# Kernel optimization log

Measured on AMD Instinct MI355X. Metric: run time of the kernel, lower is better.

Reference implementation:

```python
import jax, jax.numpy as jnp
import numpy as np

M, K, N = 131072, 512, 512


def setup_inputs() -> dict:
    key = jax.random.key(0)
    k1, k2, k3, k4 = jax.random.split(key, 4)
    # Simulated int8 quantized values held in float32 (real kernel uses int8)
    x = jnp.round(jax.random.normal(k1, (M, K), dtype=jnp.float32) * 30.0)
    weight = jnp.round(jax.random.normal(k2, (N, K), dtype=jnp.float32) * 30.0)
    # per-token activation scale [M,1], per-output-channel weight scale [N]
    x_scale = jax.random.uniform(k3, (M, 1), dtype=jnp.float32, minval=1e-3, maxval=2e-2)
    weight_scale = jax.random.uniform(k4, (N,), dtype=jnp.float32, minval=1e-3, maxval=2e-2)
    return {"x": x, "x_scale": x_scale, "weight": weight, "weight_scale": weight_scale}


def reference(x, x_scale, weight, weight_scale):
    # gemm_a8w8(per_Token): out[m,n] = (sum_k x[m,k]*W[n,k]) * x_scale[m] * w_scale[n]
    acc = jnp.einsum('mk,nk->mn', x, weight)          # [M, N] int32-equivalent accum
    out = acc * x_scale * weight_scale[None, :]       # fused dequant scaling
    return out  # otype would be bf16 in the original; kept fp32 as reference baseline
```

## Files before the change

### kernel.cpp

```cpp
#include <hip/hip_runtime.h>
#include <hip/hip_bf16.h>
#include <stdint.h>

#define K_DIM 512
#define N_DIM 512
#define BM 64
#define BN 256
#define PHASE_K 64
#define PHASE_FLOATS (BM * PHASE_K)
#define NBUF 3

typedef __bf16 bf16x8 __attribute__((ext_vector_type(8)));
typedef float floatx4 __attribute__((ext_vector_type(4)));

__device__ __forceinline__ bf16x8 cvt8(float4 a, float4 b) {
    bf16x8 r;
    r[0] = (__bf16)a.x; r[1] = (__bf16)a.y; r[2] = (__bf16)a.z; r[3] = (__bf16)a.w;
    r[4] = (__bf16)b.x; r[5] = (__bf16)b.y; r[6] = (__bf16)b.z; r[7] = (__bf16)b.w;
    return r;
}

__global__ __launch_bounds__(512) void wconv_kernel(const float* __restrict__ w,
                                                    __bf16* __restrict__ wf) {
    int t = blockIdx.x * 512 + threadIdx.x;
    int lane = t & 63, slot = t >> 6;
    int n = ((slot >> 4) << 4) + (lane & 15);
    int k = ((slot & 15) << 5) + ((lane >> 4) << 3);
    const float* src = w + (size_t)n * K_DIM + k;
    float4 f0 = *(const float4*)src;
    float4 f1 = *(const float4*)(src + 4);
    *(bf16x8*)(wf + (size_t)t * 8) = cvt8(f0, f1);
}

__device__ __forceinline__ void stage_phase(const float* __restrict__ x,
                                            int rowBase, int kBase,
                                            float* ldsBuf, int wid, int lane) {
    #pragma unroll
    for (int i = 0; i < 2; ++i) {
        int sl = i * 8 + wid;
        int row = sl * 4 + (lane >> 4);
        int srcByte = ((lane & 15) << 4) ^ ((row & 7) << 4);
        const float* g = x + (size_t)(rowBase + row) * K_DIM + kBase + (srcByte >> 2);
        float* l = ldsBuf + sl * 256;
        __builtin_amdgcn_global_load_lds(
            (const __attribute__((address_space(1))) void*)g,
            (__attribute__((address_space(3))) void*)l, 16, 0, 0);
    }
}

__device__ __forceinline__ bf16x8 read_afrag(const float* ldsBuf, int mg, int rt,
                                             int kcl, int lane) {
    int row = mg * 32 + rt * 16 + (lane & 15);
    int sw = (row & 7) << 4;
    int b0 = kcl * 128 + ((lane >> 4) << 5);
    const char* rb = (const char*)(ldsBuf + row * PHASE_K);
    float4 fa = *(const float4*)(rb + (b0 ^ sw));
    float4 fb = *(const float4*)(rb + ((b0 + 16) ^ sw));
    return cvt8(fa, fb);
}

template <bool USE_WF>
__device__ __forceinline__ void load_wfrag(bf16x8 (&dst)[4][2], int p,
                                           const __bf16* __restrict__ wf,
                                           const float* __restrict__ w,
                                           int ntgBase, int lane) {
    #pragma unroll
    for (int nt = 0; nt < 4; ++nt) {
        int ntg = ntgBase + nt;
        #pragma unroll
        for (int kcl = 0; kcl < 2; ++kcl) {
            int kcg = p * 2 + kcl;
            if (USE_WF) {
                dst[nt][kcl] = *(const bf16x8*)(wf + (size_t)(((ntg << 4) + kcg) * 64 + lane) * 8);
            } else {
                int n = (ntg << 4) + (lane & 15);
                const float* s = w + (size_t)n * K_DIM + (kcg << 5) + ((lane >> 4) << 3);
                dst[nt][kcl] = cvt8(*(const float4*)s, *(const float4*)(s + 4));
            }
        }
    }
}

template <bool USE_WF>
__global__ __launch_bounds__(512, 4) void gemm_kernel(
    const float* __restrict__ x, const float* __restrict__ xscale,
    const __bf16* __restrict__ wf, const float* __restrict__ w,
    const float* __restrict__ wscale, float* __restrict__ out)
{
    __shared__ __align__(16) float lds[NBUF * PHASE_FLOATS];
    const int t = threadIdx.x;
    const int lane = t & 63;
    const int wid = t >> 6;
    const int mg = wid >> 2;
    const int ng = wid & 3;
    const int laneR = lane & 15;

    const int bid = blockIdx.x;
    const int tile = bid >> 1;
    const int half = bid & 1;
    const int rowb = tile * BM;
    const int ntgBase = half * 16 + ng * 4;

    floatx4 acc[2][4];
    #pragma unroll
    for (int i = 0; i < 2; ++i)
        #pragma unroll
        for (int j = 0; j < 4; ++j) acc[i][j] = (floatx4)0.f;

    bf16x8 wfr[4][2];

    stage_phase(x, rowb, 0, lds, wid, lane);
    __builtin_amdgcn_sched_barrier(0);

    #pragma unroll
    for (int p = 0; p < 8; ++p) {
        load_wfrag<USE_WF>(wfr, p, wf, w, ntgBase, lane);
        __builtin_amdgcn_sched_barrier(0);

        if (p < 7) {
            stage_phase(x, rowb, (p + 1) * PHASE_K,
                        lds + ((p + 1) % NBUF) * PHASE_FLOATS, wid, lane);
            __builtin_amdgcn_sched_barrier(0);
            asm volatile("s_waitcnt vmcnt(2) lgkmcnt(0)\n\ts_barrier" ::: "memory");
        } else {
            asm volatile("s_waitcnt vmcnt(0) lgkmcnt(0)\n\ts_barrier" ::: "memory");
        }

        const float* cb = lds + (p % NBUF) * PHASE_FLOATS;
        #pragma unroll
        for (int kcl = 0; kcl < 2; ++kcl) {
            bf16x8 ax[2];
            #pragma unroll
            for (int rt = 0; rt < 2; ++rt)
                ax[rt] = read_afrag(cb, mg, rt, kcl, lane);
            #pragma unroll
            for (int nt = 0; nt < 4; ++nt)
                #pragma unroll
                for (int rt = 0; rt < 2; ++rt)
                    acc[rt][nt] = __builtin_amdgcn_mfma_f32_16x16x32_bf16(
                        wfr[nt][kcl], ax[rt], acc[rt][nt], 0, 0, 0);
        }
    }

    #pragma unroll
    for (int rt = 0; rt < 2; ++rt) {
        int m = rowb + mg * 32 + rt * 16 + laneR;
        float xs = xscale[m];
        #pragma unroll
        for (int nt = 0; nt < 4; ++nt) {
            int nb = half * BN + ng * 64 + (nt << 4) + ((lane >> 4) << 2);
            float4 wsc = *(const float4*)(wscale + nb);
            floatx4 a = acc[rt][nt];
            float4 o;
            o.x = a[0] * xs * wsc.x;
            o.y = a[1] * xs * wsc.y;
            o.z = a[2] * xs * wsc.z;
            o.w = a[3] * xs * wsc.w;
            *(float4*)(out + (size_t)m * N_DIM + nb) = o;
        }
    }
}

extern "C" void kernel_launch(void* const* d_in, const int* in_sizes, int n_in,
                              void* d_out, int out_size, void* d_ws, size_t ws_size,
                              hipStream_t stream) {
    const float* x      = (const float*)d_in[0];
    const float* xscale = (const float*)d_in[1];
    const float* w      = (const float*)d_in[2];
    const float* wscale = (const float*)d_in[3];
    float* out          = (float*)d_out;

    const int M = in_sizes[0] / K_DIM;
    const int grid = (M / BM) * 2;

    if (ws_size >= (size_t)(N_DIM * K_DIM * sizeof(unsigned short))) {
        __bf16* wfp = (__bf16*)d_ws;
        wconv_kernel<<<dim3(64), dim3(512), 0, stream>>>(w, wfp);
        gemm_kernel<true><<<dim3(grid), dim3(512), 0, stream>>>(
            x, xscale, wfp, w, wscale, out);
    } else {
        gemm_kernel<false><<<dim3(grid), dim3(512), 0, stream>>>(
            x, xscale, nullptr, w, wscale, out);
    }
}
```

Before: 217.8 us.

## Shrink N tile to 128 with 256-thread blocks and XCD-aware block remap

Halves the N tile from 256 to 128, so each block runs 4 waves and the grid doubles to four column tiles per row tile. A block-index remap keeps the four column tiles of a row tile on the same XCD so they can share the x rows in L2. The LDS pipeline goes from a triple buffer with a hand-written partial waitcnt to a double buffer guarded by __syncthreads. In exchange, x rows are read by four blocks instead of two, and the full barrier plus simpler waiting may expose more load latency.

```diff
diff --git a/kernel.cpp b/kernel.cpp
--- a/kernel.cpp
+++ b/kernel.cpp
@@ -5,10 +5,9 @@
 #define K_DIM 512
 #define N_DIM 512
 #define BM 64
-#define BN 256
+#define BN 128
 #define PHASE_K 64
 #define PHASE_FLOATS (BM * PHASE_K)
-#define NBUF 3
 
 typedef __bf16 bf16x8 __attribute__((ext_vector_type(8)));
 typedef float floatx4 __attribute__((ext_vector_type(4)));
@@ -36,8 +35,8 @@
                                             int rowBase, int kBase,
                                             float* ldsBuf, int wid, int lane) {
     #pragma unroll
-    for (int i = 0; i < 2; ++i) {
-        int sl = i * 8 + wid;
+    for (int i = 0; i < 4; ++i) {
+        int sl = i * 4 + wid;
         int row = sl * 4 + (lane >> 4);
         int srcByte = ((lane & 15) << 4) ^ ((row & 7) << 4);
         const float* g = x + (size_t)(rowBase + row) * K_DIM + kBase + (srcByte >> 2);
@@ -82,24 +81,26 @@
 }
 
 template <bool USE_WF>
-__global__ __launch_bounds__(512, 4) void gemm_kernel(
+__global__ __launch_bounds__(256, 4) void gemm_kernel(
     const float* __restrict__ x, const float* __restrict__ xscale,
     const __bf16* __restrict__ wf, const float* __restrict__ w,
-    const float* __restrict__ wscale, float* __restrict__ out)
+    const float* __restrict__ wscale, float* __restrict__ out,
+    int chunkPerXcd)
 {
-    __shared__ __align__(16) float lds[NBUF * PHASE_FLOATS];
+    __shared__ __align__(16) float lds[2 * PHASE_FLOATS];
     const int t = threadIdx.x;
     const int lane = t & 63;
     const int wid = t >> 6;
-    const int mg = wid >> 2;
-    const int ng = wid & 3;
+    const int mg = wid >> 1;
+    const int ng = wid & 1;
     const int laneR = lane & 15;
 
-    const int bid = blockIdx.x;
-    const int tile = bid >> 1;
-    const int half = bid & 1;
-    const int rowb = tile * BM;
-    const int ntgBase = half * 16 + ng * 4;
+    const int b = blockIdx.x;
+    const int L = (b & 7) * chunkPerXcd + (b >> 3);
+    const int rowTile = L >> 2;
+    const int col = L & 3;
+    const int rowb = rowTile * BM;
+    const int ntgBase = col * 8 + ng * 4;
 
     floatx4 acc[2][4];
     #pragma unroll
@@ -110,23 +111,20 @@
     bf16x8 wfr[4][2];
 
     stage_phase(x, rowb, 0, lds, wid, lane);
-    __builtin_amdgcn_sched_barrier(0);
 
     #pragma unroll
     for (int p = 0; p < 8; ++p) {
+        __syncthreads();
+
         load_wfrag<USE_WF>(wfr, p, wf, w, ntgBase, lane);
         __builtin_amdgcn_sched_barrier(0);
 
-        if (p < 7) {
+        if (p < 7)
             stage_phase(x, rowb, (p + 1) * PHASE_K,
-                        lds + ((p + 1) % NBUF) * PHASE_FLOATS, wid, lane);
-            __builtin_amdgcn_sched_barrier(0);
-            asm volatile("s_waitcnt vmcnt(2) lgkmcnt(0)\n\ts_barrier" ::: "memory");
-        } else {
-            asm volatile("s_waitcnt vmcnt(0) lgkmcnt(0)\n\ts_barrier" ::: "memory");
-        }
+                        &lds[((p + 1) & 1) * PHASE_FLOATS], wid, lane);
+        __builtin_amdgcn_sched_barrier(0);
 
-        const float* cb = lds + (p % NBUF) * PHASE_FLOATS;
+        const float* cb = &lds[(p & 1) * PHASE_FLOATS];
         #pragma unroll
         for (int kcl = 0; kcl < 2; ++kcl) {
             bf16x8 ax[2];
@@ -148,7 +146,7 @@
         float xs = xscale[m];
         #pragma unroll
         for (int nt = 0; nt < 4; ++nt) {
-            int nb = half * BN + ng * 64 + (nt << 4) + ((lane >> 4) << 2);
+            int nb = col * BN + ng * 64 + (nt << 4) + ((lane >> 4) << 2);
             float4 wsc = *(const float4*)(wscale + nb);
             floatx4 a = acc[rt][nt];
             float4 o;
@@ -171,15 +169,16 @@
     float* out          = (float*)d_out;
 
     const int M = in_sizes[0] / K_DIM;
-    const int grid = (M / BM) * 2;
+    const int grid = (M / BM) * 4;
+    const int chunkPerXcd = grid / 8;
 
     if (ws_size >= (size_t)(N_DIM * K_DIM * sizeof(unsigned short))) {
         __bf16* wfp = (__bf16*)d_ws;
         wconv_kernel<<<dim3(64), dim3(512), 0, stream>>>(w, wfp);
-        gemm_kernel<true><<<dim3(grid), dim3(512), 0, stream>>>(
-            x, xscale, wfp, w, wscale, out);
+        gemm_kernel<true><<<dim3(grid), dim3(256), 0, stream>>>(
+            x, xscale, wfp, w, wscale, out, chunkPerXcd);
     } else {
-        gemm_kernel<false><<<dim3(grid), dim3(512), 0, stream>>>(
-            x, xscale, nullptr, w, wscale, out);
+        gemm_kernel<false><<<dim3(grid), dim3(256), 0, stream>>>(
+            x, xscale, nullptr, w, wscale, out, chunkPerXcd);
     }
 }
```

Result: faster. 204.5 us (-6.1%).
